# Optimization experiments

Hardware: AMD Instinct MI355X
Metric: run time of the kernel (lower is better)

Reference implementation:

```python
import jax, jax.numpy as jnp
import numpy as np

SWIGLU_ALPHA = 1.702
SWIGLU_LIMIT = 7.0
B, S, H, E, K, I = 2, 2048, 2048, 32, 4, 1024


def setup_inputs() -> dict:
    key = jax.random.key(0)
    ks = jax.random.split(key, 8)
    return {
        "hidden_states": jax.random.normal(ks[0], (B, S, H), jnp.float32),
        "gate_w": jax.random.normal(ks[1], (E, H), jnp.float32) * 0.02,
        "gate_b": jnp.zeros((E,), jnp.float32),
        "w_gate": jax.random.normal(ks[2], (E, H, I), jnp.float32) * 0.02,
        "b_gate": jnp.zeros((E, I), jnp.float32),
        "w_up": jax.random.normal(ks[3], (E, H, I), jnp.float32) * 0.02,
        "b_up": jnp.zeros((E, I), jnp.float32),
        "w_down": jax.random.normal(ks[4], (E, I, H), jnp.float32) * 0.02,
        "b_down": jnp.zeros((E, H), jnp.float32),
    }


def reference(hidden_states, gate_w, gate_b, w_gate, b_gate, w_up, b_up, w_down, b_down):
    Bb, Ss, Hh = hidden_states.shape
    x = hidden_states.reshape(-1, Hh)                      # [T, H]
    # --- gate: top-k logits first, then softmax over the selected subset ---
    logits = x @ gate_w.T + gate_b                         # [T, E]
    topk_logits, topk_idx = jax.lax.top_k(logits, K)       # sorted descending
    topk_weight = jax.nn.softmax(topk_logits.astype(jnp.float32), axis=-1)  # [T, K]
    # --- dispatch: replicate each token K times, sort by expert id ---
    flat_idx = topk_idx.reshape(-1)                        # [T*K]
    xs = jnp.repeat(x, K, axis=0)                          # [T*K, H]
    order = jnp.argsort(flat_idx)                          # stable sort by expert
    xt = xs[order]
    gid = flat_idx[order]                                  # expert id per sorted row
    group_sizes = jnp.bincount(flat_idx, length=E).astype(jnp.int32)
    # --- grouped GEMM experts with GPT-OSS SwiGLU ---
    gate = jax.lax.ragged_dot(xt, w_gate, group_sizes) + b_gate[gid]
    up = jax.lax.ragged_dot(xt, w_up, group_sizes) + b_up[gid]
    gate = jnp.minimum(gate, SWIGLU_LIMIT)
    up = jnp.clip(up, -SWIGLU_LIMIT, SWIGLU_LIMIT)
    glu = gate * jax.nn.sigmoid(SWIGLU_ALPHA * gate)
    activated = (up + 1.0) * glu
    outs = jax.lax.ragged_dot(activated, w_down, group_sizes) + b_down[gid]
    # --- unsort and combine with routing weights ---
    inv = jnp.argsort(order)
    outs = outs[inv].reshape(-1, K, Hh)                    # [T, K, H]
    y = jnp.sum(outs * topk_weight[..., None], axis=1).astype(x.dtype)
    return y.reshape(Bb, Ss, Hh)
```

## Files before the change

kernel.cpp:

```cpp
#include <hip/hip_runtime.h>

#define T_TOK 4096
#define E_EXP 32
#define KSEL  4
#define HDIM  2048
#define IDIM  1024
#define TKROW 16384
#define BM    128

typedef __attribute__((ext_vector_type(8))) short   short8;
typedef __attribute__((ext_vector_type(8))) __bf16  bf16x8;
typedef __attribute__((ext_vector_type(4))) float   f32x4;

static __device__ __forceinline__ f32x4 mfma16(short8 a, short8 b, f32x4 c) {
    return __builtin_amdgcn_mfma_f32_16x16x32_bf16(
        __builtin_bit_cast(bf16x8, a), __builtin_bit_cast(bf16x8, b), c, 0, 0, 0);
}

static __device__ __forceinline__ unsigned short f2bf(float f) {
    unsigned u = __builtin_bit_cast(unsigned, f);
    unsigned r = (u + 0x7FFFu + ((u >> 16) & 1u)) >> 16;
    return (unsigned short)r;
}
static __device__ __forceinline__ float bf2f(unsigned short u) {
    return __builtin_bit_cast(float, ((unsigned)u) << 16);
}
static __device__ __forceinline__ unsigned cvtpk(float lo, float hi) {
    unsigned r;
    asm("v_cvt_pk_bf16_f32 %0, %1, %2" : "=v"(r) : "v"(lo), "v"(hi));
    return r;
}

__global__ __launch_bounds__(256) void gating_kernel(
    const float* __restrict__ x, const float* __restrict__ gw,
    const float* __restrict__ gb, int* __restrict__ topk_idx,
    float* __restrict__ topk_w)
{
    int wave = threadIdx.x >> 6, lane = threadIdx.x & 63;
    int t = blockIdx.x * 4 + wave;
    const float* xr = x + (size_t)t * HDIM;
    float xv[32];
#pragma unroll
    for (int j = 0; j < 32; j++) xv[j] = xr[lane + 64 * j];
    float logits[E_EXP];
#pragma unroll
    for (int e = 0; e < E_EXP; e++) {
        const float* wr = gw + (size_t)e * HDIM;
        float s = 0.f;
#pragma unroll
        for (int j = 0; j < 32; j++) s = fmaf(xv[j], wr[lane + 64 * j], s);
#pragma unroll
        for (int off = 32; off; off >>= 1) s += __shfl_xor(s, off);
        logits[e] = s + gb[e];
    }
    unsigned sel = 0;
    float v[4]; int id[4];
#pragma unroll
    for (int kk = 0; kk < 4; kk++) {
        float best = -3.4e38f; int bi = 0;
#pragma unroll
        for (int e = 0; e < E_EXP; e++) {
            bool ok = ((sel >> e) & 1u) == 0u;
            bool gt = ok && (logits[e] > best);
            best = gt ? logits[e] : best;
            bi   = gt ? e : bi;
        }
        sel |= 1u << bi; v[kk] = best; id[kk] = bi;
    }
    float m0 = v[0];
    float e0 = __expf(v[0] - m0), e1 = __expf(v[1] - m0);
    float e2 = __expf(v[2] - m0), e3 = __expf(v[3] - m0);
    float inv = 1.f / (e0 + e1 + e2 + e3);
    if (lane == 0) {
        int b4 = t * 4;
        topk_idx[b4 + 0] = id[0]; topk_w[b4 + 0] = e0 * inv;
        topk_idx[b4 + 1] = id[1]; topk_w[b4 + 1] = e1 * inv;
        topk_idx[b4 + 2] = id[2]; topk_w[b4 + 2] = e2 * inv;
        topk_idx[b4 + 3] = id[3]; topk_w[b4 + 3] = e3 * inv;
    }
}

__global__ void init_kernel(int* counts, int* fill) {
    if (threadIdx.x < E_EXP) { counts[threadIdx.x] = 0; fill[threadIdx.x] = 0; }
}

__global__ void histo_kernel(const int* __restrict__ idx, int* counts) {
    int i = blockIdx.x * 256 + threadIdx.x;
    atomicAdd(&counts[idx[i]], 1);
}

__global__ void scan_tiles_kernel(const int* counts, int* offsets,
                                  int* tile_e, int* tile_r, int* ntiles) {
    if (threadIdx.x == 0) {
        int acc = 0;
        for (int e = 0; e < E_EXP; e++) { offsets[e] = acc; acc += counts[e]; }
        offsets[E_EXP] = acc;
        int nt = 0;
        for (int e = 0; e < E_EXP; e++) {
            int c = counts[e];
            for (int r = 0; r < c; r += BM) {
                tile_e[nt] = e; tile_r[nt] = offsets[e] + r; nt++;
            }
        }
        ntiles[0] = nt;
    }
}

__global__ void scatter_kernel(const int* __restrict__ idx, const int* __restrict__ offsets,
                               int* fill, int* __restrict__ pos_of, int* __restrict__ row_tok) {
    int i = blockIdx.x * 256 + threadIdx.x;
    int e = idx[i];
    int pos = offsets[e] + atomicAdd(&fill[e], 1);
    pos_of[i] = pos;
    row_tok[pos] = i >> 2;
}

__global__ __launch_bounds__(64) void gather_kernel(
    const float* __restrict__ x, const int* __restrict__ row_tok,
    unsigned short* __restrict__ xt)
{
    int r = blockIdx.x, lane = threadIdx.x;
    const f32x4* src = (const f32x4*)(x + (size_t)row_tok[r] * HDIM);
    unsigned short* dst = xt + (size_t)r * HDIM;
#pragma unroll
    for (int j = 0; j < 8; j++) {
        f32x4 f = src[lane + 64 * j];
        uint2 o;
        o.x = cvtpk(f[0], f[1]);
        o.y = cvtpk(f[2], f[3]);
        *(uint2*)(dst + 4 * (lane + 64 * j)) = o;
    }
}

__global__ __launch_bounds__(256, 2) void gemm1_kernel(
    const unsigned short* __restrict__ xt, const float* __restrict__ w_gate,
    const float* __restrict__ b_gate, const float* __restrict__ w_up,
    const float* __restrict__ b_up, const int* __restrict__ tile_e,
    const int* __restrict__ tile_r, const int* __restrict__ ntiles,
    const int* __restrict__ offsets, const int* __restrict__ counts,
    unsigned short* __restrict__ act)
{
    int tid = blockIdx.y;
    if (tid >= ntiles[0]) return;
    int e = tile_e[tid], row0 = tile_r[tid];
    int cnt_end = offsets[e] + counts[e];
    int n0 = blockIdx.x * 64;
    __shared__ unsigned short As[128 * 64];
    __shared__ unsigned short Bg[64 * 64];
    __shared__ unsigned short Bu[64 * 64];
    int t = threadIdx.x, lane = t & 63, wave = t >> 6;
    int wr = wave >> 1, wc = wave & 1;
    f32x4 accg[4][2], accu[4][2];
#pragma unroll
    for (int m = 0; m < 4; m++)
#pragma unroll
        for (int n = 0; n < 2; n++) { accg[m][n] = (f32x4)0.f; accu[m][n] = (f32x4)0.f; }

    int arow = t >> 1, akh = (t & 1) * 32;
    int asr = row0 + arow; if (asr > TKROW - 1) asr = TKROW - 1;
    const unsigned short* ap = xt + (size_t)asr * HDIM + akh;
    int aw  = arow * 64 + akh;
    int axk = ((arow >> 2) & 3) << 4;
    int bn = (t & 15) * 4, bk = (t >> 4) * 4;
    size_t wbase = (size_t)e * ((size_t)HDIM * IDIM) + (size_t)bk * IDIM + n0 + bn;
    const float* gp = w_gate + wbase;
    const float* upp = w_up + wbase;
    int bxk = (t & 3) << 4;
    int lrow = lane & 15, lg8 = (lane >> 4) * 8;
    int rxk = ((lrow >> 2) & 3) << 4;

    short8 aR[4]; f32x4 gR[4], uR[4];
#define LOAD_T1() do { \
    aR[0] = *(const short8*)(ap);      aR[1] = *(const short8*)(ap + 8);  \
    aR[2] = *(const short8*)(ap + 16); aR[3] = *(const short8*)(ap + 24); \
    gR[0] = *(const f32x4*)(gp);                 gR[1] = *(const f32x4*)(gp + IDIM);      \
    gR[2] = *(const f32x4*)(gp + 2 * IDIM);      gR[3] = *(const f32x4*)(gp + 3 * IDIM);  \
    uR[0] = *(const f32x4*)(upp);                uR[1] = *(const f32x4*)(upp + IDIM);     \
    uR[2] = *(const f32x4*)(upp + 2 * IDIM);     uR[3] = *(const f32x4*)(upp + 3 * IDIM); \
    ap += 64; gp += (size_t)64 * IDIM; upp += (size_t)64 * IDIM; } while (0)

    LOAD_T1();
    for (int k0 = 0; k0 < HDIM; k0 += 64) {
        __syncthreads();
#pragma unroll
        for (int j = 0; j < 4; j++)
            *(short8*)&As[(aw + 8 * j) ^ axk] = aR[j];
#pragma unroll
        for (int j = 0; j < 4; j++) {
            uint2 vg, vu;
            vg.x = cvtpk(gR[0][j], gR[1][j]); vg.y = cvtpk(gR[2][j], gR[3][j]);
            vu.x = cvtpk(uR[0][j], uR[1][j]); vu.y = cvtpk(uR[2][j], uR[3][j]);
            int r = bn + j;
            *(uint2*)&Bg[(r * 64 + bk) ^ bxk] = vg;
            *(uint2*)&Bu[(r * 64 + bk) ^ bxk] = vu;
        }
        if (k0 + 64 < HDIM) LOAD_T1();
        __syncthreads();
#pragma unroll
        for (int kk = 0; kk < 2; kk++) {
            short8 af[4], bgf[2], buf2[2];
#pragma unroll
            for (int m = 0; m < 4; m++)
                af[m] = *(const short8*)&As[((wr * 64 + m * 16 + lrow) * 64 + kk * 32 + lg8) ^ rxk];
#pragma unroll
            for (int n = 0; n < 2; n++) {
                int rb = (wc * 32 + n * 16 + lrow) * 64 + kk * 32 + lg8;
                bgf[n]  = *(const short8*)&Bg[rb ^ rxk];
                buf2[n] = *(const short8*)&Bu[rb ^ rxk];
            }
#pragma unroll
            for (int m = 0; m < 4; m++)
#pragma unroll
                for (int n = 0; n < 2; n++) {
                    accg[m][n] = mfma16(af[m], bgf[n], accg[m][n]);
                    accu[m][n] = mfma16(af[m], buf2[n], accu[m][n]);
                }
        }
    }
#undef LOAD_T1
#pragma unroll
    for (int n = 0; n < 2; n++) {
        int gcol = n0 + wc * 32 + n * 16 + lrow;
        float bgv = b_gate[e * IDIM + gcol];
        float buv = b_up[e * IDIM + gcol];
#pragma unroll
        for (int m = 0; m < 4; m++) {
            int rb = row0 + wr * 64 + m * 16 + (lane >> 4) * 4;
#pragma unroll
            for (int r = 0; r < 4; r++) {
                int grow = rb + r;
                if (grow < cnt_end) {
                    float gv = accg[m][n][r] + bgv;
                    float uv = accu[m][n][r] + buv;
                    gv = fminf(gv, 7.f);
                    uv = fminf(fmaxf(uv, -7.f), 7.f);
                    float glu = gv / (1.f + __expf(-1.702f * gv));
                    float av = (uv + 1.f) * glu;
                    act[(size_t)grow * IDIM + gcol] = f2bf(av);
                }
            }
        }
    }
}

__global__ __launch_bounds__(256, 2) void gemm2_kernel(
    const unsigned short* __restrict__ act, const float* __restrict__ w_down,
    const float* __restrict__ b_down, const int* __restrict__ tile_e,
    const int* __restrict__ tile_r, const int* __restrict__ ntiles,
    const int* __restrict__ offsets, const int* __restrict__ counts,
    unsigned short* __restrict__ outs)
{
    int tid = blockIdx.y;
    if (tid >= ntiles[0]) return;
    int e = tile_e[tid], row0 = tile_r[tid];
    int cnt_end = offsets[e] + counts[e];
    int n0 = blockIdx.x * 64;
    __shared__ unsigned short As[128 * 64];
    __shared__ unsigned short Bs[64 * 64];
    int t = threadIdx.x, lane = t & 63, wave = t >> 6;
    int wr = wave >> 1, wc = wave & 1;
    f32x4 acc[4][2];
#pragma unroll
    for (int m = 0; m < 4; m++)
#pragma unroll
        for (int n = 0; n < 2; n++) acc[m][n] = (f32x4)0.f;

    int arow = t >> 1, akh = (t & 1) * 32;
    int asr = row0 + arow; if (asr > TKROW - 1) asr = TKROW - 1;
    const unsigned short* ap = act + (size_t)asr * IDIM + akh;
    int aw  = arow * 64 + akh;
    int axk = ((arow >> 2) & 3) << 4;
    int bn = (t & 15) * 4, bk = (t >> 4) * 4;
    const float* gp = w_down + (size_t)e * ((size_t)IDIM * HDIM) + (size_t)bk * HDIM + n0 + bn;
    int bxk = (t & 3) << 4;
    int lrow = lane & 15, lg8 = (lane >> 4) * 8;
    int rxk = ((lrow >> 2) & 3) << 4;

    short8 aR[4]; f32x4 gR[4];
#define LOAD_T2() do { \
    aR[0] = *(const short8*)(ap);      aR[1] = *(const short8*)(ap + 8);  \
    aR[2] = *(const short8*)(ap + 16); aR[3] = *(const short8*)(ap + 24); \
    gR[0] = *(const f32x4*)(gp);                 gR[1] = *(const f32x4*)(gp + HDIM);      \
    gR[2] = *(const f32x4*)(gp + 2 * HDIM);      gR[3] = *(const f32x4*)(gp + 3 * HDIM);  \
    ap += 64; gp += (size_t)64 * HDIM; } while (0)

    LOAD_T2();
    for (int k0 = 0; k0 < IDIM; k0 += 64) {
        __syncthreads();
#pragma unroll
        for (int j = 0; j < 4; j++)
            *(short8*)&As[(aw + 8 * j) ^ axk] = aR[j];
#pragma unroll
        for (int j = 0; j < 4; j++) {
            uint2 vg;
            vg.x = cvtpk(gR[0][j], gR[1][j]); vg.y = cvtpk(gR[2][j], gR[3][j]);
            int r = bn + j;
            *(uint2*)&Bs[(r * 64 + bk) ^ bxk] = vg;
        }
        if (k0 + 64 < IDIM) LOAD_T2();
        __syncthreads();
#pragma unroll
        for (int kk = 0; kk < 2; kk++) {
            short8 af[4], bf[2];
#pragma unroll
            for (int m = 0; m < 4; m++)
                af[m] = *(const short8*)&As[((wr * 64 + m * 16 + lrow) * 64 + kk * 32 + lg8) ^ rxk];
#pragma unroll
            for (int n = 0; n < 2; n++)
                bf[n] = *(const short8*)&Bs[((wc * 32 + n * 16 + lrow) * 64 + kk * 32 + lg8) ^ rxk];
#pragma unroll
            for (int m = 0; m < 4; m++)
#pragma unroll
                for (int n = 0; n < 2; n++)
                    acc[m][n] = mfma16(af[m], bf[n], acc[m][n]);
        }
    }
#undef LOAD_T2
#pragma unroll
    for (int n = 0; n < 2; n++) {
        int gcol = n0 + wc * 32 + n * 16 + lrow;
        float bdv = b_down[e * HDIM + gcol];
#pragma unroll
        for (int m = 0; m < 4; m++) {
            int rb = row0 + wr * 64 + m * 16 + (lane >> 4) * 4;
#pragma unroll
            for (int r = 0; r < 4; r++) {
                int grow = rb + r;
                if (grow < cnt_end)
                    outs[(size_t)grow * HDIM + gcol] = f2bf(acc[m][n][r] + bdv);
            }
        }
    }
}

__global__ __launch_bounds__(256) void combine_kernel(
    const unsigned short* __restrict__ outs, const int* __restrict__ pos_of,
    const float* __restrict__ topk_w, float* __restrict__ y)
{
    int tok = blockIdx.x;
    int c0 = threadIdx.x * 8;
    float acc[8] = {0.f, 0.f, 0.f, 0.f, 0.f, 0.f, 0.f, 0.f};
#pragma unroll
    for (int k = 0; k < 4; k++) {
        int pos = pos_of[tok * 4 + k];
        float w = topk_w[tok * 4 + k];
        short8 vv = *(const short8*)(outs + (size_t)pos * HDIM + c0);
#pragma unroll
        for (int j = 0; j < 8; j++)
            acc[j] = fmaf(w, bf2f((unsigned short)vv[j]), acc[j]);
    }
    float4 o0 = make_float4(acc[0], acc[1], acc[2], acc[3]);
    float4 o1 = make_float4(acc[4], acc[5], acc[6], acc[7]);
    *(float4*)(y + (size_t)tok * HDIM + c0)     = o0;
    *(float4*)(y + (size_t)tok * HDIM + c0 + 4) = o1;
}

extern "C" void kernel_launch(void* const* d_in, const int* in_sizes, int n_in,
                              void* d_out, int out_size, void* d_ws, size_t ws_size,
                              hipStream_t stream) {
    const float* x      = (const float*)d_in[0];
    const float* gw     = (const float*)d_in[1];
    const float* gb     = (const float*)d_in[2];
    const float* w_gate = (const float*)d_in[3];
    const float* b_gate = (const float*)d_in[4];
    const float* w_up   = (const float*)d_in[5];
    const float* b_up   = (const float*)d_in[6];
    const float* w_down = (const float*)d_in[7];
    const float* b_down = (const float*)d_in[8];
    float* y = (float*)d_out;

    char* base = (char*)d_ws;
    size_t off = 0;
    int*   topk_idx = (int*)(base + off);   off += (size_t)TKROW * 4;
    float* topk_w   = (float*)(base + off); off += (size_t)TKROW * 4;
    int*   counts   = (int*)(base + off);   off += 256;
    int*   offsets  = (int*)(base + off);   off += 256;
    int*   fill     = (int*)(base + off);   off += 256;
    int*   ntiles   = (int*)(base + off);   off += 256;
    int*   tile_e   = (int*)(base + off);   off += 1024;
    int*   tile_r   = (int*)(base + off);   off += 1024;
    int*   pos_of   = (int*)(base + off);   off += (size_t)TKROW * 4;
    int*   row_tok  = (int*)(base + off);   off += (size_t)TKROW * 4;
    unsigned short* xt   = (unsigned short*)(base + off); off += (size_t)TKROW * HDIM * 2;
    unsigned short* act  = (unsigned short*)(base + off); off += (size_t)TKROW * IDIM * 2;
    unsigned short* outs = (unsigned short*)(base + off); off += (size_t)TKROW * HDIM * 2;

    init_kernel<<<1, 64, 0, stream>>>(counts, fill);
    gating_kernel<<<T_TOK / 4, 256, 0, stream>>>(x, gw, gb, topk_idx, topk_w);
    histo_kernel<<<TKROW / 256, 256, 0, stream>>>(topk_idx, counts);
    scan_tiles_kernel<<<1, 64, 0, stream>>>(counts, offsets, tile_e, tile_r, ntiles);
    scatter_kernel<<<TKROW / 256, 256, 0, stream>>>(topk_idx, offsets, fill, pos_of, row_tok);
    gather_kernel<<<TKROW, 64, 0, stream>>>(x, row_tok, xt);
    gemm1_kernel<<<dim3(IDIM / 64, 160), 256, 0, stream>>>(
        xt, w_gate, b_gate, w_up, b_up, tile_e, tile_r, ntiles, offsets, counts, act);
    gemm2_kernel<<<dim3(HDIM / 64, 160), 256, 0, stream>>>(
        act, w_down, b_down, tile_e, tile_r, ntiles, offsets, counts, outs);
    combine_kernel<<<T_TOK, 256, 0, stream>>>(outs, pos_of, topk_w, y);
}
```

Before: 686.0 us.

## Double-buffer LDS with two-deep register prefetch in expert GEMM kernels

Both grouped GEMM kernels now use ping-pong LDS buffers with two register prefetch stages, so each iteration needs one barrier instead of two and global loads overlap MFMA work more deeply. The LDS swizzle moves to an 8-way XOR on row bits, and MFMA sections raise wave priority with s_setprio. gemm2 now requests 3 blocks per SM in its launch bounds. The cost is double LDS use and more live registers, which may cut occupancy or cause spills.

```diff
diff --git a/kernel.cpp b/kernel.cpp
--- a/kernel.cpp
+++ b/kernel.cpp
@@ -30,6 +30,12 @@
     asm("v_cvt_pk_bf16_f32 %0, %1, %2" : "=v"(r) : "v"(lo), "v"(hi));
     return r;
 }
+
+#define BARRIER() do { \
+    asm volatile("s_waitcnt lgkmcnt(0)" ::: "memory"); \
+    __builtin_amdgcn_s_barrier(); \
+    __builtin_amdgcn_sched_barrier(0); \
+} while (0)
 
 __global__ __launch_bounds__(256) void gating_kernel(
     const float* __restrict__ x, const float* __restrict__ gw,
@@ -145,9 +151,9 @@
     int e = tile_e[tid], row0 = tile_r[tid];
     int cnt_end = offsets[e] + counts[e];
     int n0 = blockIdx.x * 64;
-    __shared__ unsigned short As[128 * 64];
-    __shared__ unsigned short Bg[64 * 64];
-    __shared__ unsigned short Bu[64 * 64];
+    __shared__ unsigned short As[2][128 * 64];
+    __shared__ unsigned short Bg[2][64 * 64];
+    __shared__ unsigned short Bu[2][64 * 64];
     int t = threadIdx.x, lane = t & 63, wave = t >> 6;
     int wr = wave >> 1, wc = wave & 1;
     f32x4 accg[4][2], accu[4][2];
@@ -158,66 +164,85 @@
 
     int arow = t >> 1, akh = (t & 1) * 32;
     int asr = row0 + arow; if (asr > TKROW - 1) asr = TKROW - 1;
-    const unsigned short* ap = xt + (size_t)asr * HDIM + akh;
-    int aw  = arow * 64 + akh;
-    int axk = ((arow >> 2) & 3) << 4;
+    const unsigned short* apb = xt + (size_t)asr * HDIM + akh;
+    int aswz = (arow & 7) << 3;
     int bn = (t & 15) * 4, bk = (t >> 4) * 4;
     size_t wbase = (size_t)e * ((size_t)HDIM * IDIM) + (size_t)bk * IDIM + n0 + bn;
-    const float* gp = w_gate + wbase;
-    const float* upp = w_up + wbase;
-    int bxk = (t & 3) << 4;
+    const float* gpb = w_gate + wbase;
+    const float* upb = w_up + wbase;
     int lrow = lane & 15, lg8 = (lane >> 4) * 8;
-    int rxk = ((lrow >> 2) & 3) << 4;
-
-    short8 aR[4]; f32x4 gR[4], uR[4];
-#define LOAD_T1() do { \
-    aR[0] = *(const short8*)(ap);      aR[1] = *(const short8*)(ap + 8);  \
-    aR[2] = *(const short8*)(ap + 16); aR[3] = *(const short8*)(ap + 24); \
-    gR[0] = *(const f32x4*)(gp);                 gR[1] = *(const f32x4*)(gp + IDIM);      \
-    gR[2] = *(const f32x4*)(gp + 2 * IDIM);      gR[3] = *(const f32x4*)(gp + 3 * IDIM);  \
-    uR[0] = *(const f32x4*)(upp);                uR[1] = *(const f32x4*)(upp + IDIM);     \
-    uR[2] = *(const f32x4*)(upp + 2 * IDIM);     uR[3] = *(const f32x4*)(upp + 3 * IDIM); \
-    ap += 64; gp += (size_t)64 * IDIM; upp += (size_t)64 * IDIM; } while (0)
-
-    LOAD_T1();
-    for (int k0 = 0; k0 < HDIM; k0 += 64) {
-        __syncthreads();
-#pragma unroll
-        for (int j = 0; j < 4; j++)
-            *(short8*)&As[(aw + 8 * j) ^ axk] = aR[j];
-#pragma unroll
-        for (int j = 0; j < 4; j++) {
-            uint2 vg, vu;
-            vg.x = cvtpk(gR[0][j], gR[1][j]); vg.y = cvtpk(gR[2][j], gR[3][j]);
-            vu.x = cvtpk(uR[0][j], uR[1][j]); vu.y = cvtpk(uR[2][j], uR[3][j]);
-            int r = bn + j;
-            *(uint2*)&Bg[(r * 64 + bk) ^ bxk] = vg;
-            *(uint2*)&Bu[(r * 64 + bk) ^ bxk] = vu;
-        }
-        if (k0 + 64 < HDIM) LOAD_T1();
-        __syncthreads();
-#pragma unroll
-        for (int kk = 0; kk < 2; kk++) {
-            short8 af[4], bgf[2], buf2[2];
-#pragma unroll
-            for (int m = 0; m < 4; m++)
-                af[m] = *(const short8*)&As[((wr * 64 + m * 16 + lrow) * 64 + kk * 32 + lg8) ^ rxk];
-#pragma unroll
-            for (int n = 0; n < 2; n++) {
-                int rb = (wc * 32 + n * 16 + lrow) * 64 + kk * 32 + lg8;
-                bgf[n]  = *(const short8*)&Bg[rb ^ rxk];
-                buf2[n] = *(const short8*)&Bu[rb ^ rxk];
-            }
-#pragma unroll
-            for (int m = 0; m < 4; m++)
-#pragma unroll
-                for (int n = 0; n < 2; n++) {
-                    accg[m][n] = mfma16(af[m], bgf[n], accg[m][n]);
-                    accu[m][n] = mfma16(af[m], buf2[n], accu[m][n]);
-                }
-        }
-    }
-#undef LOAD_T1
+    int rswz = (lane & 7) << 3;
+
+    short8 a0[4], a1[4]; f32x4 g0[4], g1[4], u0[4], u1[4];
+
+#define G1_ISSUE(aD, gD, uD, KT) do { int kt_ = (KT); \
+    const unsigned short* ax_ = apb + (size_t)kt_ * 64; \
+    aD[0] = *(const short8*)(ax_);      aD[1] = *(const short8*)(ax_ + 8);  \
+    aD[2] = *(const short8*)(ax_ + 16); aD[3] = *(const short8*)(ax_ + 24); \
+    const float* gx_ = gpb + (size_t)kt_ * (64 * IDIM); \
+    const float* ux_ = upb + (size_t)kt_ * (64 * IDIM); \
+    gD[0] = *(const f32x4*)(gx_);            gD[1] = *(const f32x4*)(gx_ + IDIM);     \
+    gD[2] = *(const f32x4*)(gx_ + 2 * IDIM); gD[3] = *(const f32x4*)(gx_ + 3 * IDIM); \
+    uD[0] = *(const f32x4*)(ux_);            uD[1] = *(const f32x4*)(ux_ + IDIM);     \
+    uD[2] = *(const f32x4*)(ux_ + 2 * IDIM); uD[3] = *(const f32x4*)(ux_ + 3 * IDIM); \
+} while (0)
+
+#define G1_WRITE(aS, gS, uS, DST) do { \
+    unsigned short* Ad_ = &As[DST][0]; \
+    unsigned short* Bgd_ = &Bg[DST][0]; unsigned short* Bud_ = &Bu[DST][0]; \
+    _Pragma("unroll") for (int j = 0; j < 4; j++) \
+        *(short8*)&Ad_[arow * 64 + ((akh + 8 * j) ^ aswz)] = aS[j]; \
+    _Pragma("unroll") for (int j = 0; j < 4; j++) { \
+        uint2 vg_, vu_; \
+        vg_.x = cvtpk(gS[0][j], gS[1][j]); vg_.y = cvtpk(gS[2][j], gS[3][j]); \
+        vu_.x = cvtpk(uS[0][j], uS[1][j]); vu_.y = cvtpk(uS[2][j], uS[3][j]); \
+        int r_ = bn + j; int d_ = r_ * 64 + (bk ^ ((r_ & 7) << 3)); \
+        *(uint2*)&Bgd_[d_] = vg_; *(uint2*)&Bud_[d_] = vu_; \
+    } \
+} while (0)
+
+#define G1_MFMA(P) do { \
+    const unsigned short* Ab_ = &As[P][0]; \
+    const unsigned short* Bgb_ = &Bg[P][0]; const unsigned short* Bub_ = &Bu[P][0]; \
+    __builtin_amdgcn_s_setprio(1); \
+    _Pragma("unroll") for (int kk = 0; kk < 2; kk++) { \
+        short8 af_[4], bg_[2], bu_[2]; \
+        int ke_ = (kk * 32 + lg8) ^ rswz; \
+        _Pragma("unroll") for (int m = 0; m < 4; m++) { \
+            int rr_ = wr * 64 + m * 16 + lrow; \
+            af_[m] = *(const short8*)&Ab_[rr_ * 64 + ke_]; } \
+        _Pragma("unroll") for (int n = 0; n < 2; n++) { \
+            int rr_ = wc * 32 + n * 16 + lrow; \
+            bg_[n] = *(const short8*)&Bgb_[rr_ * 64 + ke_]; \
+            bu_[n] = *(const short8*)&Bub_[rr_ * 64 + ke_]; } \
+        _Pragma("unroll") for (int m = 0; m < 4; m++) \
+        _Pragma("unroll") for (int n = 0; n < 2; n++) { \
+            accg[m][n] = mfma16(af_[m], bg_[n], accg[m][n]); \
+            accu[m][n] = mfma16(af_[m], bu_[n], accu[m][n]); } \
+    } \
+    __builtin_amdgcn_s_setprio(0); \
+} while (0)
+
+    G1_ISSUE(a0, g0, u0, 0);
+    G1_ISSUE(a1, g1, u1, 1);
+    G1_WRITE(a0, g0, u0, 0);
+    G1_ISSUE(a0, g0, u0, 2);
+    BARRIER();
+    int p = 0;
+    for (int kt = 0; kt < 32; kt += 2) {
+        if (kt + 1 < 32) G1_WRITE(a1, g1, u1, p ^ 1);
+        if (kt + 3 < 32) G1_ISSUE(a1, g1, u1, kt + 3);
+        G1_MFMA(p);
+        BARRIER(); p ^= 1;
+        if (kt + 2 < 32) G1_WRITE(a0, g0, u0, p ^ 1);
+        if (kt + 4 < 32) G1_ISSUE(a0, g0, u0, kt + 4);
+        G1_MFMA(p);
+        BARRIER(); p ^= 1;
+    }
+#undef G1_ISSUE
+#undef G1_WRITE
+#undef G1_MFMA
+
 #pragma unroll
     for (int n = 0; n < 2; n++) {
         int gcol = n0 + wc * 32 + n * 16 + lrow;
@@ -243,7 +268,7 @@
     }
 }
 
-__global__ __launch_bounds__(256, 2) void gemm2_kernel(
+__global__ __launch_bounds__(256, 3) void gemm2_kernel(
     const unsigned short* __restrict__ act, const float* __restrict__ w_down,
     const float* __restrict__ b_down, const int* __restrict__ tile_e,
     const int* __restrict__ tile_r, const int* __restrict__ ntiles,
@@ -255,8 +280,8 @@
     int e = tile_e[tid], row0 = tile_r[tid];
     int cnt_end = offsets[e] + counts[e];
     int n0 = blockIdx.x * 64;
-    __shared__ unsigned short As[128 * 64];
-    __shared__ unsigned short Bs[64 * 64];
+    __shared__ unsigned short As[2][128 * 64];
+    __shared__ unsigned short Bs[2][64 * 64];
     int t = threadIdx.x, lane = t & 63, wave = t >> 6;
     int wr = wave >> 1, wc = wave & 1;
     f32x4 acc[4][2];
@@ -267,55 +292,75 @@
 
     int arow = t >> 1, akh = (t & 1) * 32;
     int asr = row0 + arow; if (asr > TKROW - 1) asr = TKROW - 1;
-    const unsigned short* ap = act + (size_t)asr * IDIM + akh;
-    int aw  = arow * 64 + akh;
-    int axk = ((arow >> 2) & 3) << 4;
+    const unsigned short* apb = act + (size_t)asr * IDIM + akh;
+    int aswz = (arow & 7) << 3;
     int bn = (t & 15) * 4, bk = (t >> 4) * 4;
-    const float* gp = w_down + (size_t)e * ((size_t)IDIM * HDIM) + (size_t)bk * HDIM + n0 + bn;
-    int bxk = (t & 3) << 4;
+    const float* gpb = w_down + (size_t)e * ((size_t)IDIM * HDIM) + (size_t)bk * HDIM + n0 + bn;
     int lrow = lane & 15, lg8 = (lane >> 4) * 8;
-    int rxk = ((lrow >> 2) & 3) << 4;
-
-    short8 aR[4]; f32x4 gR[4];
-#define LOAD_T2() do { \
-    aR[0] = *(const short8*)(ap);      aR[1] = *(const short8*)(ap + 8);  \
-    aR[2] = *(const short8*)(ap + 16); aR[3] = *(const short8*)(ap + 24); \
-    gR[0] = *(const f32x4*)(gp);                 gR[1] = *(const f32x4*)(gp + HDIM);      \
-    gR[2] = *(const f32x4*)(gp + 2 * HDIM);      gR[3] = *(const f32x4*)(gp + 3 * HDIM);  \
-    ap += 64; gp += (size_t)64 * HDIM; } while (0)
-
-    LOAD_T2();
-    for (int k0 = 0; k0 < IDIM; k0 += 64) {
-        __syncthreads();
-#pragma unroll
-        for (int j = 0; j < 4; j++)
-            *(short8*)&As[(aw + 8 * j) ^ axk] = aR[j];
-#pragma unroll
-        for (int j = 0; j < 4; j++) {
-            uint2 vg;
-            vg.x = cvtpk(gR[0][j], gR[1][j]); vg.y = cvtpk(gR[2][j], gR[3][j]);
-            int r = bn + j;
-            *(uint2*)&Bs[(r * 64 + bk) ^ bxk] = vg;
-        }
-        if (k0 + 64 < IDIM) LOAD_T2();
-        __syncthreads();
-#pragma unroll
-        for (int kk = 0; kk < 2; kk++) {
-            short8 af[4], bf[2];
-#pragma unroll
-            for (int m = 0; m < 4; m++)
-                af[m] = *(const short8*)&As[((wr * 64 + m * 16 + lrow) * 64 + kk * 32 + lg8) ^ rxk];
-#pragma unroll
-            for (int n = 0; n < 2; n++)
-                bf[n] = *(const short8*)&Bs[((wc * 32 + n * 16 + lrow) * 64 + kk * 32 + lg8) ^ rxk];
-#pragma unroll
-            for (int m = 0; m < 4; m++)
-#pragma unroll
-                for (int n = 0; n < 2; n++)
-                    acc[m][n] = mfma16(af[m], bf[n], acc[m][n]);
-        }
-    }
-#undef LOAD_T2
+    int rswz = (lane & 7) << 3;
+
+    short8 a0[4], a1[4]; f32x4 g0[4], g1[4];
+
+#define G2_ISSUE(aD, gD, KT) do { int kt_ = (KT); \
+    const unsigned short* ax_ = apb + (size_t)kt_ * 64; \
+    aD[0] = *(const short8*)(ax_);      aD[1] = *(const short8*)(ax_ + 8);  \
+    aD[2] = *(const short8*)(ax_ + 16); aD[3] = *(const short8*)(ax_ + 24); \
+    const float* gx_ = gpb + (size_t)kt_ * (64 * HDIM); \
+    gD[0] = *(const f32x4*)(gx_);            gD[1] = *(const f32x4*)(gx_ + HDIM);     \
+    gD[2] = *(const f32x4*)(gx_ + 2 * HDIM); gD[3] = *(const f32x4*)(gx_ + 3 * HDIM); \
+} while (0)
+
+#define G2_WRITE(aS, gS, DST) do { \
+    unsigned short* Ad_ = &As[DST][0]; unsigned short* Bd_ = &Bs[DST][0]; \
+    _Pragma("unroll") for (int j = 0; j < 4; j++) \
+        *(short8*)&Ad_[arow * 64 + ((akh + 8 * j) ^ aswz)] = aS[j]; \
+    _Pragma("unroll") for (int j = 0; j < 4; j++) { \
+        uint2 vg_; \
+        vg_.x = cvtpk(gS[0][j], gS[1][j]); vg_.y = cvtpk(gS[2][j], gS[3][j]); \
+        int r_ = bn + j; int d_ = r_ * 64 + (bk ^ ((r_ & 7) << 3)); \
+        *(uint2*)&Bd_[d_] = vg_; \
+    } \
+} while (0)
+
+#define G2_MFMA(P) do { \
+    const unsigned short* Ab_ = &As[P][0]; const unsigned short* Bb_ = &Bs[P][0]; \
+    __builtin_amdgcn_s_setprio(1); \
+    _Pragma("unroll") for (int kk = 0; kk < 2; kk++) { \
+        short8 af_[4], bf_[2]; \
+        int ke_ = (kk * 32 + lg8) ^ rswz; \
+        _Pragma("unroll") for (int m = 0; m < 4; m++) { \
+            int rr_ = wr * 64 + m * 16 + lrow; \
+            af_[m] = *(const short8*)&Ab_[rr_ * 64 + ke_]; } \
+        _Pragma("unroll") for (int n = 0; n < 2; n++) { \
+            int rr_ = wc * 32 + n * 16 + lrow; \
+            bf_[n] = *(const short8*)&Bb_[rr_ * 64 + ke_]; } \
+        _Pragma("unroll") for (int m = 0; m < 4; m++) \
+        _Pragma("unroll") for (int n = 0; n < 2; n++) \
+            acc[m][n] = mfma16(af_[m], bf_[n], acc[m][n]); \
+    } \
+    __builtin_amdgcn_s_setprio(0); \
+} while (0)
+
+    G2_ISSUE(a0, g0, 0);
+    G2_ISSUE(a1, g1, 1);
+    G2_WRITE(a0, g0, 0);
+    G2_ISSUE(a0, g0, 2);
+    BARRIER();
+    int p = 0;
+    for (int kt = 0; kt < 16; kt += 2) {
+        if (kt + 1 < 16) G2_WRITE(a1, g1, p ^ 1);
+        if (kt + 3 < 16) G2_ISSUE(a1, g1, kt + 3);
+        G2_MFMA(p);
+        BARRIER(); p ^= 1;
+        if (kt + 2 < 16) G2_WRITE(a0, g0, p ^ 1);
+        if (kt + 4 < 16) G2_ISSUE(a0, g0, kt + 4);
+        G2_MFMA(p);
+        BARRIER(); p ^= 1;
+    }
+#undef G2_ISSUE
+#undef G2_WRITE
+#undef G2_MFMA
+
 #pragma unroll
     for (int n = 0; n < 2; n++) {
         int gcol = n0 + wc * 32 + n * 16 + lrow;
```

Result: no change. 672.8 us (-1.9%).

## Enlarge expert GEMM tiles and double-buffer LDS with direct global-to-LDS loads

Applied to the files above, without the earlier changes.

Both grouped GEMMs move from 128x64 tiles with 256 threads to 256-row tiles with 512 threads. GEMM1 now covers 128 columns and GEMM2 covers 256 columns. Shared memory is double-buffered, A tiles are loaded straight into LDS via global_load_lds, and MFMA sections run at raised wave priority. Launches use a swizzled flat block index over a fixed maximum of 96 tiles. The larger M tiles reduce how often the fp32 expert weights are re-read and converted, and the pipeline overlaps loads with compute. In exchange, each kernel uses about 128KB of LDS, which limits occupancy, and ragged expert groups waste more padded rows.

```diff
diff --git a/kernel.cpp b/kernel.cpp
--- a/kernel.cpp
+++ b/kernel.cpp
@@ -2,15 +2,22 @@
 
 #define T_TOK 4096
 #define E_EXP 32
-#define KSEL  4
 #define HDIM  2048
 #define IDIM  1024
 #define TKROW 16384
-#define BM    128
+#define BM    256
+#define MAXT  96
 
 typedef __attribute__((ext_vector_type(8))) short   short8;
 typedef __attribute__((ext_vector_type(8))) __bf16  bf16x8;
 typedef __attribute__((ext_vector_type(4))) float   f32x4;
+
+typedef const __attribute__((address_space(1))) unsigned int* gas_t;
+typedef __attribute__((address_space(3))) unsigned int*       las_t;
+
+static __device__ __forceinline__ void gload16(const void* g, void* l) {
+    __builtin_amdgcn_global_load_lds((gas_t)(uintptr_t)g, (las_t)(uintptr_t)l, 16, 0, 0);
+}
 
 static __device__ __forceinline__ f32x4 mfma16(short8 a, short8 b, f32x4 c) {
     return __builtin_amdgcn_mfma_f32_16x16x32_bf16(
@@ -30,6 +37,9 @@
     asm("v_cvt_pk_bf16_f32 %0, %1, %2" : "=v"(r) : "v"(lo), "v"(hi));
     return r;
 }
+
+#define VM0()   asm volatile("s_waitcnt vmcnt(0)" ::: "memory")
+#define LGKM0() asm volatile("s_waitcnt lgkmcnt(0)" ::: "memory")
 
 __global__ __launch_bounds__(256) void gating_kernel(
     const float* __restrict__ x, const float* __restrict__ gw,
@@ -132,7 +142,7 @@
     }
 }
 
-__global__ __launch_bounds__(256, 2) void gemm1_kernel(
+__global__ __launch_bounds__(512, 2) void gemm1_kernel(
     const unsigned short* __restrict__ xt, const float* __restrict__ w_gate,
     const float* __restrict__ b_gate, const float* __restrict__ w_up,
     const float* __restrict__ b_up, const int* __restrict__ tile_e,
@@ -140,194 +150,240 @@
     const int* __restrict__ offsets, const int* __restrict__ counts,
     unsigned short* __restrict__ act)
 {
-    int tid = blockIdx.y;
+    int flat = blockIdx.y * 8 + blockIdx.x;
+    int swz = (flat & 7) * (MAXT * 8 / 8) + (flat >> 3);
+    int tid = swz >> 3, nb = swz & 7;
     if (tid >= ntiles[0]) return;
     int e = tile_e[tid], row0 = tile_r[tid];
     int cnt_end = offsets[e] + counts[e];
-    int n0 = blockIdx.x * 64;
-    __shared__ unsigned short As[128 * 64];
-    __shared__ unsigned short Bg[64 * 64];
-    __shared__ unsigned short Bu[64 * 64];
-    int t = threadIdx.x, lane = t & 63, wave = t >> 6;
-    int wr = wave >> 1, wc = wave & 1;
-    f32x4 accg[4][2], accu[4][2];
-#pragma unroll
-    for (int m = 0; m < 4; m++)
+    int n0 = nb * 128;
+
+    __shared__ unsigned short As[2][BM * 64];
+    __shared__ unsigned short Bgs[2][128 * 64];
+    __shared__ unsigned short Bus[2][128 * 64];
+
+    int t = threadIdx.x, lane = t & 63, w = t >> 6;
+    int wr = w >> 2, wc = w & 3;
+    int lrow = lane & 15, lg8 = (lane >> 4) * 8;
+
+    f32x4 accg[8][2], accu[8][2];
+#pragma unroll
+    for (int m = 0; m < 8; m++)
 #pragma unroll
         for (int n = 0; n < 2; n++) { accg[m][n] = (f32x4)0.f; accu[m][n] = (f32x4)0.f; }
 
-    int arow = t >> 1, akh = (t & 1) * 32;
-    int asr = row0 + arow; if (asr > TKROW - 1) asr = TKROW - 1;
-    const unsigned short* ap = xt + (size_t)asr * HDIM + akh;
-    int aw  = arow * 64 + akh;
-    int axk = ((arow >> 2) & 3) << 4;
-    int bn = (t & 15) * 4, bk = (t >> 4) * 4;
-    size_t wbase = (size_t)e * ((size_t)HDIM * IDIM) + (size_t)bk * IDIM + n0 + bn;
-    const float* gp = w_gate + wbase;
-    const float* upp = w_up + wbase;
-    int bxk = (t & 3) << 4;
-    int lrow = lane & 15, lg8 = (lane >> 4) * 8;
-    int rxk = ((lrow >> 2) & 3) << 4;
-
-    short8 aR[4]; f32x4 gR[4], uR[4];
-#define LOAD_T1() do { \
-    aR[0] = *(const short8*)(ap);      aR[1] = *(const short8*)(ap + 8);  \
-    aR[2] = *(const short8*)(ap + 16); aR[3] = *(const short8*)(ap + 24); \
-    gR[0] = *(const f32x4*)(gp);                 gR[1] = *(const f32x4*)(gp + IDIM);      \
-    gR[2] = *(const f32x4*)(gp + 2 * IDIM);      gR[3] = *(const f32x4*)(gp + 3 * IDIM);  \
-    uR[0] = *(const f32x4*)(upp);                uR[1] = *(const f32x4*)(upp + IDIM);     \
-    uR[2] = *(const f32x4*)(upp + 2 * IDIM);     uR[3] = *(const f32x4*)(upp + 3 * IDIM); \
-    ap += 64; gp += (size_t)64 * IDIM; upp += (size_t)64 * IDIM; } while (0)
-
-    LOAD_T1();
-    for (int k0 = 0; k0 < HDIM; k0 += 64) {
-        __syncthreads();
-#pragma unroll
-        for (int j = 0; j < 4; j++)
-            *(short8*)&As[(aw + 8 * j) ^ axk] = aR[j];
-#pragma unroll
-        for (int j = 0; j < 4; j++) {
-            uint2 vg, vu;
-            vg.x = cvtpk(gR[0][j], gR[1][j]); vg.y = cvtpk(gR[2][j], gR[3][j]);
-            vu.x = cvtpk(uR[0][j], uR[1][j]); vu.y = cvtpk(uR[2][j], uR[3][j]);
-            int r = bn + j;
-            *(uint2*)&Bg[(r * 64 + bk) ^ bxk] = vg;
-            *(uint2*)&Bu[(r * 64 + bk) ^ bxk] = vu;
-        }
-        if (k0 + 64 < HDIM) LOAD_T1();
-        __syncthreads();
-#pragma unroll
-        for (int kk = 0; kk < 2; kk++) {
-            short8 af[4], bgf[2], buf2[2];
-#pragma unroll
-            for (int m = 0; m < 4; m++)
-                af[m] = *(const short8*)&As[((wr * 64 + m * 16 + lrow) * 64 + kk * 32 + lg8) ^ rxk];
-#pragma unroll
-            for (int n = 0; n < 2; n++) {
-                int rb = (wc * 32 + n * 16 + lrow) * 64 + kk * 32 + lg8;
-                bgf[n]  = *(const short8*)&Bg[rb ^ rxk];
-                buf2[n] = *(const short8*)&Bu[rb ^ rxk];
-            }
-#pragma unroll
-            for (int m = 0; m < 4; m++)
-#pragma unroll
-                for (int n = 0; n < 2; n++) {
-                    accg[m][n] = mfma16(af[m], bgf[n], accg[m][n]);
-                    accu[m][n] = mfma16(af[m], buf2[n], accu[m][n]);
-                }
-        }
-    }
-#undef LOAD_T1
-#pragma unroll
-    for (int n = 0; n < 2; n++) {
-        int gcol = n0 + wc * 32 + n * 16 + lrow;
-        float bgv = b_gate[e * IDIM + gcol];
-        float buv = b_up[e * IDIM + gcol];
-#pragma unroll
-        for (int m = 0; m < 4; m++) {
-            int rb = row0 + wr * 64 + m * 16 + (lane >> 4) * 4;
+    int arow_l = (lane >> 3);
+    int achunk = (lane & 7) ^ arow_l;
+    int bn = (t & 31) * 4, bk = (t >> 5) * 4;
+    int bfswz = ((t & 31) & 7) << 3;
+    size_t wB = (size_t)e * ((size_t)HDIM * IDIM) + (size_t)bk * IDIM + n0 + bn;
+
+    f32x4 gReg[4], uReg[4];
+
+#define G1_STAGE_A(KT, BUF) do { int k0_ = (KT) * 64; \
+    _Pragma("unroll") for (int i_ = 0; i_ < 4; i_++) { \
+        int ar_ = row0 + 32 * w + 8 * i_ + arow_l; \
+        if (ar_ > TKROW - 1) ar_ = TKROW - 1; \
+        gload16(xt + (size_t)ar_ * HDIM + k0_ + achunk * 8, \
+                (void*)&As[BUF][(32 * w + 8 * i_) * 64]); \
+    } } while (0)
+
+#define G1_LOADB(KT) do { \
+    const float* gp_ = w_gate + wB + (size_t)(KT) * 64 * IDIM; \
+    const float* up_ = w_up   + wB + (size_t)(KT) * 64 * IDIM; \
+    _Pragma("unroll") for (int kk_ = 0; kk_ < 4; kk_++) { \
+        gReg[kk_] = *(const f32x4*)(gp_ + (size_t)kk_ * IDIM); \
+        uReg[kk_] = *(const f32x4*)(up_ + (size_t)kk_ * IDIM); \
+    } } while (0)
+
+#define G1_WRITEB(BUF) do { \
+    _Pragma("unroll") for (int j_ = 0; j_ < 4; j_++) { \
+        uint2 vg_, vu_; \
+        vg_.x = cvtpk(gReg[0][j_], gReg[1][j_]); vg_.y = cvtpk(gReg[2][j_], gReg[3][j_]); \
+        vu_.x = cvtpk(uReg[0][j_], uReg[1][j_]); vu_.y = cvtpk(uReg[2][j_], uReg[3][j_]); \
+        int d_ = (bn + j_) * 64 + (bk ^ bfswz); \
+        *(uint2*)&Bgs[BUF][d_] = vg_; *(uint2*)&Bus[BUF][d_] = vu_; \
+    } } while (0)
+
+#define G1_MFMA(BUF) do { \
+    __builtin_amdgcn_s_setprio(1); \
+    _Pragma("unroll") for (int kk_ = 0; kk_ < 2; kk_++) { \
+        short8 af_[8], bg_[2], bu_[2]; \
+        int ke_ = kk_ * 32 + lg8; \
+        _Pragma("unroll") for (int m_ = 0; m_ < 8; m_++) \
+            af_[m_] = *(const short8*)&As[BUF][(wr * 128 + m_ * 16 + lrow) * 64 + (ke_ ^ ((lrow & 7) << 3))]; \
+        _Pragma("unroll") for (int n_ = 0; n_ < 2; n_++) { \
+            int rb_ = wc * 32 + n_ * 16 + lrow; \
+            int d_ = rb_ * 64 + (ke_ ^ (((rb_ >> 2) & 7) << 3)); \
+            bg_[n_] = *(const short8*)&Bgs[BUF][d_]; \
+            bu_[n_] = *(const short8*)&Bus[BUF][d_]; \
+        } \
+        _Pragma("unroll") for (int m_ = 0; m_ < 8; m_++) \
+        _Pragma("unroll") for (int n_ = 0; n_ < 2; n_++) { \
+            accg[m_][n_] = mfma16(af_[m_], bg_[n_], accg[m_][n_]); \
+            accu[m_][n_] = mfma16(af_[m_], bu_[n_], accu[m_][n_]); \
+        } \
+    } \
+    __builtin_amdgcn_s_setprio(0); } while (0)
+
+    G1_STAGE_A(0, 0);
+    G1_LOADB(0);
+    VM0();
+    G1_WRITEB(0);
+    LGKM0();
+    __builtin_amdgcn_s_barrier();
+
+    int cur = 0;
+#pragma unroll 1
+    for (int kt = 0; kt < 32; kt++) {
+        if (kt + 1 < 32) { G1_STAGE_A(kt + 1, cur ^ 1); G1_LOADB(kt + 1); }
+        G1_MFMA(cur);
+        VM0();
+        if (kt + 1 < 32) G1_WRITEB(cur ^ 1);
+        LGKM0();
+        __builtin_amdgcn_s_barrier();
+        cur ^= 1;
+    }
+#undef G1_STAGE_A
+#undef G1_LOADB
+#undef G1_WRITEB
+#undef G1_MFMA
+
+#pragma unroll
+    for (int nf = 0; nf < 2; nf++) {
+        int col = n0 + wc * 32 + nf * 16 + lrow;
+        float bgv = b_gate[e * IDIM + col];
+        float buv = b_up[e * IDIM + col];
+#pragma unroll
+        for (int m = 0; m < 8; m++) {
+            int rb = row0 + wr * 128 + m * 16 + (lane >> 4) * 4;
 #pragma unroll
             for (int r = 0; r < 4; r++) {
                 int grow = rb + r;
                 if (grow < cnt_end) {
-                    float gv = accg[m][n][r] + bgv;
-                    float uv = accu[m][n][r] + buv;
+                    float gv = accg[m][nf][r] + bgv;
+                    float uv = accu[m][nf][r] + buv;
                     gv = fminf(gv, 7.f);
                     uv = fminf(fmaxf(uv, -7.f), 7.f);
                     float glu = gv / (1.f + __expf(-1.702f * gv));
-                    float av = (uv + 1.f) * glu;
-                    act[(size_t)grow * IDIM + gcol] = f2bf(av);
+                    act[(size_t)grow * IDIM + col] = f2bf((uv + 1.f) * glu);
                 }
             }
         }
     }
 }
 
-__global__ __launch_bounds__(256, 2) void gemm2_kernel(
-    const unsigned short* __restrict__ act, const float* __restrict__ w_down,
+__global__ __launch_bounds__(512, 2) void gemm2_kernel(
+    const unsigned short* __restrict__ actb, const float* __restrict__ w_down,
     const float* __restrict__ b_down, const int* __restrict__ tile_e,
     const int* __restrict__ tile_r, const int* __restrict__ ntiles,
     const int* __restrict__ offsets, const int* __restrict__ counts,
     unsigned short* __restrict__ outs)
 {
-    int tid = blockIdx.y;
+    int flat = blockIdx.y * 8 + blockIdx.x;
+    int swz = (flat & 7) * (MAXT * 8 / 8) + (flat >> 3);
+    int tid = swz >> 3, nb = swz & 7;
     if (tid >= ntiles[0]) return;
     int e = tile_e[tid], row0 = tile_r[tid];
     int cnt_end = offsets[e] + counts[e];
-    int n0 = blockIdx.x * 64;
-    __shared__ unsigned short As[128 * 64];
-    __shared__ unsigned short Bs[64 * 64];
-    int t = threadIdx.x, lane = t & 63, wave = t >> 6;
-    int wr = wave >> 1, wc = wave & 1;
-    f32x4 acc[4][2];
-#pragma unroll
-    for (int m = 0; m < 4; m++)
-#pragma unroll
-        for (int n = 0; n < 2; n++) acc[m][n] = (f32x4)0.f;
-
-    int arow = t >> 1, akh = (t & 1) * 32;
-    int asr = row0 + arow; if (asr > TKROW - 1) asr = TKROW - 1;
-    const unsigned short* ap = act + (size_t)asr * IDIM + akh;
-    int aw  = arow * 64 + akh;
-    int axk = ((arow >> 2) & 3) << 4;
-    int bn = (t & 15) * 4, bk = (t >> 4) * 4;
-    const float* gp = w_down + (size_t)e * ((size_t)IDIM * HDIM) + (size_t)bk * HDIM + n0 + bn;
-    int bxk = (t & 3) << 4;
+    int n0 = nb * 256;
+
+    __shared__ unsigned short As[2][BM * 64];
+    __shared__ unsigned short Bs[2][256 * 64];
+
+    int t = threadIdx.x, lane = t & 63, w = t >> 6;
+    int wr = w >> 2, wc = w & 3;
     int lrow = lane & 15, lg8 = (lane >> 4) * 8;
-    int rxk = ((lrow >> 2) & 3) << 4;
-
-    short8 aR[4]; f32x4 gR[4];
-#define LOAD_T2() do { \
-    aR[0] = *(const short8*)(ap);      aR[1] = *(const short8*)(ap + 8);  \
-    aR[2] = *(const short8*)(ap + 16); aR[3] = *(const short8*)(ap + 24); \
-    gR[0] = *(const f32x4*)(gp);                 gR[1] = *(const f32x4*)(gp + HDIM);      \
-    gR[2] = *(const f32x4*)(gp + 2 * HDIM);      gR[3] = *(const f32x4*)(gp + 3 * HDIM);  \
-    ap += 64; gp += (size_t)64 * HDIM; } while (0)
-
-    LOAD_T2();
-    for (int k0 = 0; k0 < IDIM; k0 += 64) {
-        __syncthreads();
-#pragma unroll
-        for (int j = 0; j < 4; j++)
-            *(short8*)&As[(aw + 8 * j) ^ axk] = aR[j];
-#pragma unroll
-        for (int j = 0; j < 4; j++) {
-            uint2 vg;
-            vg.x = cvtpk(gR[0][j], gR[1][j]); vg.y = cvtpk(gR[2][j], gR[3][j]);
-            int r = bn + j;
-            *(uint2*)&Bs[(r * 64 + bk) ^ bxk] = vg;
-        }
-        if (k0 + 64 < IDIM) LOAD_T2();
-        __syncthreads();
-#pragma unroll
-        for (int kk = 0; kk < 2; kk++) {
-            short8 af[4], bf[2];
-#pragma unroll
-            for (int m = 0; m < 4; m++)
-                af[m] = *(const short8*)&As[((wr * 64 + m * 16 + lrow) * 64 + kk * 32 + lg8) ^ rxk];
-#pragma unroll
-            for (int n = 0; n < 2; n++)
-                bf[n] = *(const short8*)&Bs[((wc * 32 + n * 16 + lrow) * 64 + kk * 32 + lg8) ^ rxk];
-#pragma unroll
-            for (int m = 0; m < 4; m++)
-#pragma unroll
-                for (int n = 0; n < 2; n++)
-                    acc[m][n] = mfma16(af[m], bf[n], acc[m][n]);
-        }
-    }
-#undef LOAD_T2
-#pragma unroll
-    for (int n = 0; n < 2; n++) {
-        int gcol = n0 + wc * 32 + n * 16 + lrow;
-        float bdv = b_down[e * HDIM + gcol];
-#pragma unroll
-        for (int m = 0; m < 4; m++) {
-            int rb = row0 + wr * 64 + m * 16 + (lane >> 4) * 4;
+
+    f32x4 acc[8][4];
+#pragma unroll
+    for (int m = 0; m < 8; m++)
+#pragma unroll
+        for (int n = 0; n < 4; n++) acc[m][n] = (f32x4)0.f;
+
+    int arow_l = (lane >> 3);
+    int achunk = (lane & 7) ^ arow_l;
+    int bn = (t & 63) * 4, bk = w * 8;
+    int bfswz = (lane & 7) << 3;
+    size_t wB = (size_t)e * ((size_t)IDIM * HDIM) + (size_t)bk * HDIM + n0 + bn;
+
+    f32x4 dReg[8];
+
+#define G2_STAGE_A(KT, BUF) do { int k0_ = (KT) * 64; \
+    _Pragma("unroll") for (int i_ = 0; i_ < 4; i_++) { \
+        int ar_ = row0 + 32 * w + 8 * i_ + arow_l; \
+        if (ar_ > TKROW - 1) ar_ = TKROW - 1; \
+        gload16(actb + (size_t)ar_ * IDIM + k0_ + achunk * 8, \
+                (void*)&As[BUF][(32 * w + 8 * i_) * 64]); \
+    } } while (0)
+
+#define G2_LOADB(KT) do { \
+    const float* gp_ = w_down + wB + (size_t)(KT) * 64 * HDIM; \
+    _Pragma("unroll") for (int kk_ = 0; kk_ < 8; kk_++) \
+        dReg[kk_] = *(const f32x4*)(gp_ + (size_t)kk_ * HDIM); \
+    } while (0)
+
+#define G2_WRITEB(BUF) do { \
+    _Pragma("unroll") for (int j_ = 0; j_ < 4; j_++) { \
+        uint4 v_; \
+        v_.x = cvtpk(dReg[0][j_], dReg[1][j_]); v_.y = cvtpk(dReg[2][j_], dReg[3][j_]); \
+        v_.z = cvtpk(dReg[4][j_], dReg[5][j_]); v_.w = cvtpk(dReg[6][j_], dReg[7][j_]); \
+        int d_ = (bn + j_) * 64 + (bk ^ bfswz); \
+        *(uint4*)&Bs[BUF][d_] = v_; \
+    } } while (0)
+
+#define G2_MFMA(BUF) do { \
+    __builtin_amdgcn_s_setprio(1); \
+    _Pragma("unroll") for (int kk_ = 0; kk_ < 2; kk_++) { \
+        short8 af_[8], bf_[4]; \
+        int ke_ = kk_ * 32 + lg8; \
+        _Pragma("unroll") for (int m_ = 0; m_ < 8; m_++) \
+            af_[m_] = *(const short8*)&As[BUF][(wr * 128 + m_ * 16 + lrow) * 64 + (ke_ ^ ((lrow & 7) << 3))]; \
+        _Pragma("unroll") for (int n_ = 0; n_ < 4; n_++) { \
+            int rb_ = wc * 64 + n_ * 16 + lrow; \
+            bf_[n_] = *(const short8*)&Bs[BUF][rb_ * 64 + (ke_ ^ (((rb_ >> 2) & 7) << 3))]; \
+        } \
+        _Pragma("unroll") for (int m_ = 0; m_ < 8; m_++) \
+        _Pragma("unroll") for (int n_ = 0; n_ < 4; n_++) \
+            acc[m_][n_] = mfma16(af_[m_], bf_[n_], acc[m_][n_]); \
+    } \
+    __builtin_amdgcn_s_setprio(0); } while (0)
+
+    G2_STAGE_A(0, 0);
+    G2_LOADB(0);
+    VM0();
+    G2_WRITEB(0);
+    LGKM0();
+    __builtin_amdgcn_s_barrier();
+
+    int cur = 0;
+#pragma unroll 1
+    for (int kt = 0; kt < 16; kt++) {
+        if (kt + 1 < 16) { G2_STAGE_A(kt + 1, cur ^ 1); G2_LOADB(kt + 1); }
+        G2_MFMA(cur);
+        VM0();
+        if (kt + 1 < 16) G2_WRITEB(cur ^ 1);
+        LGKM0();
+        __builtin_amdgcn_s_barrier();
+        cur ^= 1;
+    }
+#undef G2_STAGE_A
+#undef G2_LOADB
+#undef G2_WRITEB
+#undef G2_MFMA
+
+#pragma unroll
+    for (int nf = 0; nf < 4; nf++) {
+        int col = n0 + wc * 64 + nf * 16 + lrow;
+        float bdv = b_down[e * HDIM + col];
+#pragma unroll
+        for (int m = 0; m < 8; m++) {
+            int rb = row0 + wr * 128 + m * 16 + (lane >> 4) * 4;
 #pragma unroll
             for (int r = 0; r < 4; r++) {
                 int grow = rb + r;
                 if (grow < cnt_end)
-                    outs[(size_t)grow * HDIM + gcol] = f2bf(acc[m][n][r] + bdv);
+                    outs[(size_t)grow * HDIM + col] = f2bf(acc[m][nf][r] + bdv);
             }
         }
     }
@@ -391,9 +447,9 @@
     scan_tiles_kernel<<<1, 64, 0, stream>>>(counts, offsets, tile_e, tile_r, ntiles);
     scatter_kernel<<<TKROW / 256, 256, 0, stream>>>(topk_idx, offsets, fill, pos_of, row_tok);
     gather_kernel<<<TKROW, 64, 0, stream>>>(x, row_tok, xt);
-    gemm1_kernel<<<dim3(IDIM / 64, 160), 256, 0, stream>>>(
+    gemm1_kernel<<<dim3(8, MAXT), 512, 0, stream>>>(
         xt, w_gate, b_gate, w_up, b_up, tile_e, tile_r, ntiles, offsets, counts, act);
-    gemm2_kernel<<<dim3(HDIM / 64, 160), 256, 0, stream>>>(
+    gemm2_kernel<<<dim3(8, MAXT), 512, 0, stream>>>(
         act, w_down, b_down, tile_e, tile_r, ntiles, offsets, counts, outs);
     combine_kernel<<<T_TOK, 256, 0, stream>>>(outs, pos_of, topk_w, y);
 }
```

Measured after the change: 622.6 us. -9.2%, faster.
